# Kernel tuning notes

Hardware: AMD Instinct MI355X
Metric: run time of the kernel (lower is better)

The kernel has to match this reference:

```python
import jax, jax.numpy as jnp
import numpy as np

B, L, IN, D, H = 128, 64, 2, 256, 512  # batch, max_len, input_size, dense_size, hidden_size
A_S2S, A_PTR = H, D  # attention hidden sizes (defaults: hidden_size / dense_size)


def setup_inputs() -> dict:
    key = jax.random.key(0)
    ks = jax.random.split(key, 24)
    s = 0.05
    inp = {
        'inputs': jax.random.normal(ks[0], (B, L, IN), jnp.float32),
        'lengths': jax.random.randint(ks[1], (B,), L // 2, L + 1),
        'targets': jax.random.randint(ks[2], (B, L), 0, L),
        # input_dense: input_size -> dense_size
        'W_in': jax.random.normal(ks[3], (D, IN)) * s,
        'b_in': jnp.zeros((D,)),
        # encoder GRU (input D, hidden H), PyTorch layout [3H, in]
        'enc_Wi': jax.random.normal(ks[4], (3 * H, D)) * s,
        'enc_Wh': jax.random.normal(ks[5], (3 * H, H)) * s,
        'enc_bi': jnp.zeros((3 * H,)),
        'enc_bh': jnp.zeros((3 * H,)),
        # decoder GRU (input D+H, hidden H)
        'dec_Wi': jax.random.normal(ks[6], (3 * H, D + H)) * s,
        'dec_Wh': jax.random.normal(ks[7], (3 * H, H)) * s,
        'dec_bi': jnp.zeros((3 * H,)),
        'dec_bh': jnp.zeros((3 * H,)),
        # Bahdanau seq2seq attention: query_hidden = rnn_layers*H
        's2s_Wq': jax.random.normal(ks[8], (H, A_S2S)) * s,
        's2s_Wk': jax.random.normal(ks[9], (H, A_S2S)) * s,
        's2s_v': jax.random.normal(ks[10], (A_S2S,)) * s,
        # output_dense: hidden -> dense
        'W_out': jax.random.normal(ks[11], (D, H)) * s,
        'b_out': jnp.zeros((D,)),
        # Bahdanau pointer attention over dense_inputs
        'ptr_Wq': jax.random.normal(ks[12], (D, A_PTR)) * s,
        'ptr_Wk': jax.random.normal(ks[13], (D, A_PTR)) * s,
        'ptr_v': jax.random.normal(ks[14], (A_PTR,)) * s,
    }
    return inp


def _gru_cell(x, h, Wi, Wh, bi, bh):
    gi = x @ Wi.T + bi
    gh = h @ Wh.T + bh
    i_r, i_z, i_n = jnp.split(gi, 3, axis=-1)
    h_r, h_z, h_n = jnp.split(gh, 3, axis=-1)
    r = jax.nn.sigmoid(i_r + h_r)
    z = jax.nn.sigmoid(i_z + h_z)
    n = jnp.tanh(i_n + r * h_n)
    return (1.0 - z) * n + z * h


NEG = -1e9


def reference(inputs, lengths, targets, W_in, b_in, enc_Wi, enc_Wh, enc_bi, enc_bh,
              dec_Wi, dec_Wh, dec_bi, dec_bh, s2s_Wq, s2s_Wk, s2s_v,
              W_out, b_out, ptr_Wq, ptr_Wk, ptr_v):
    # teacher_forcing_prob fixed at 1.0 for determinism (uses targets each step)
    dense_inputs = inputs @ W_in.T + b_in            # [B, L, D]
    padding_mask = jnp.arange(L)[None, :] < lengths[:, None]  # [B, L] bool

    # ---- encoder (dynamic_rnn): run GRU over time, take hidden at lengths-1 ----
    def enc_step(h, x_t):
        h2 = _gru_cell(x_t, h, enc_Wi, enc_Wh, enc_bi, enc_bh)
        return h2, h2
    _, hs = jax.lax.scan(enc_step, jnp.zeros((B, H), dense_inputs.dtype),
                         dense_inputs.transpose(1, 0, 2))  # hs: [L, B, H]
    enc_out = hs.transpose(1, 0, 2) * padding_mask[:, :, None]  # zero padded steps
    hidden0 = hs[lengths - 1, jnp.arange(B)]  # final valid hidden, [B, H]

    # Precompute attention key projections (loop-invariant)
    enc_keys = enc_out @ s2s_Wk        # [B, L, A_S2S]
    ptr_keys = dense_inputs @ ptr_Wk   # [B, L, A_PTR]

    def dec_step(carry, inp):
        h, idx, step_mask = carry              # h [B,H], idx [B] int, step_mask [B,L]
        pm_i, tgt_i = inp                      # [B] bool, [B] int
        dec_in = dense_inputs[jnp.arange(B), idx]  # [B, D] gather
        m = pm_i[:, None] & padding_mask           # [B, L]
        # Bahdanau seq2seq attention, query = current hidden state
        q = h @ s2s_Wq                              # [B, A]
        scores = jnp.tanh(q[:, None, :] + enc_keys) @ s2s_v   # [B, L]
        scores = jnp.where(m, scores, NEG)
        w = jax.nn.softmax(scores, axis=-1)
        context = jnp.einsum('bl,blh->bh', w, enc_out)         # [B, H]
        x = jnp.concatenate([context, dec_in], axis=-1)        # [B, H+D]
        h_new = _gru_cell(x, h, dec_Wi, dec_Wh, dec_bi, dec_bh)
        # pointer attention over dense_inputs
        dense_out = h_new @ W_out.T + b_out                    # [B, D]
        p_mask = (step_mask > 0) & m
        pq = dense_out @ ptr_Wq
        plogit = jnp.tanh(pq[:, None, :] + ptr_keys) @ ptr_v   # [B, L]
        plogit = jnp.where(p_mask, plogit, NEG)
        pred = jnp.argmax(plogit, axis=-1)
        next_idx = tgt_i  # teacher forcing
        step_mask_new = step_mask * (1 - jax.nn.one_hot(next_idx, L, dtype=step_mask.dtype))
        return (h_new, next_idx, step_mask_new), (plogit, pred)

    carry0 = (hidden0, jnp.zeros((B,), jnp.int32),
              jnp.ones((B, L), jnp.int32))
    xs = (padding_mask.T, targets.T.astype(jnp.int32))
    _, (logits_t, preds_t) = jax.lax.scan(dec_step, carry0, xs)
    logits = logits_t.transpose(1, 0, 2)       # [B, L, L]
    predictions = preds_t.T                    # [B, L]
    return logits, predictions
```

## Files before the change

kernel.cpp:

```cpp
#include <hip/hip_runtime.h>

#define BB 128
#define LL 64
#define DD 256
#define HH 512
#define NEGC (-1e9f)

#define OFF_DENSE   0
#define OFF_ENCOUT  2097152
#define OFF_ENCKEYS 6291456
#define OFF_PTRKEYS 10485760
#define OFF_X       12582912
#define OFF_HB0     12681216
#define OFF_HB1     12746752
#define OFF_H0      12812288
#define OFF_Q       12877824
#define OFF_PQ      12943360
#define OFF_WQT     12976128
#define OFF_MT      13238272
#define OFF_BQ      13369344
#define OFF_SMASK   13369600

__device__ __forceinline__ float fast_tanh(float x) {
  float e = __expf(2.0f * x);
  return 1.0f - 2.0f / (e + 1.0f);
}
__device__ __forceinline__ float sigmoidf_(float x) {
  return 1.0f / (1.0f + __expf(-x));
}
__device__ __forceinline__ float wsum(float v) {
#pragma unroll
  for (int o = 32; o > 0; o >>= 1) v += __shfl_xor(v, o);
  return v;
}

#define D4(acc) fmaf(xv.x, w.x, fmaf(xv.y, w.y, fmaf(xv.z, w.z, fmaf(xv.w, w.w, acc))))


__global__ __launch_bounds__(256)
void k_init(const float* __restrict__ inp, const float* __restrict__ W_in,
            const float* __restrict__ b_in, float* __restrict__ dense,
            float* __restrict__ hb0, int* __restrict__ smask) {
  int idx = blockIdx.x * 256 + threadIdx.x;
  if (idx < BB * LL * DD) {
    int bl = idx >> 8, d = idx & 255;
    dense[idx] = fmaf(inp[bl * 2], W_in[d * 2], fmaf(inp[bl * 2 + 1], W_in[d * 2 + 1], b_in[d]));
  } else if (idx < BB * LL * DD + BB * HH) {
    hb0[idx - BB * LL * DD] = 0.f;
  } else if (idx < BB * LL * DD + BB * HH + BB * LL) {
    smask[idx - BB * LL * DD - BB * HH] = 1;
  }
}

__global__ __launch_bounds__(256)
void k_tr(const float* __restrict__ Wq, float* __restrict__ Wqt) {
  int idx = blockIdx.x * 256 + threadIdx.x;
  int h = idx >> 9, a = idx & 511;
  Wqt[a * 512 + h] = Wq[idx];
}

__global__ __launch_bounds__(512)
void k_mt(const float* __restrict__ W_out, const float* __restrict__ ptr_Wq,
          const float* __restrict__ b_out, float* __restrict__ Mt, float* __restrict__ bqv) {
  int a = blockIdx.x, tid = threadIdx.x;
  if (a < 256) {
    float acc = 0.f;
    for (int d = 0; d < 256; ++d) acc = fmaf(W_out[d * 512 + tid], ptr_Wq[d * 256 + a], acc);
    Mt[a * 512 + tid] = acc;
  } else if (tid < 256) {
    float acc = 0.f;
    for (int d = 0; d < 256; ++d) acc = fmaf(b_out[d], ptr_Wq[d * 256 + tid], acc);
    bqv[tid] = acc;
  }
}

__global__ __launch_bounds__(256)
void k_ptrkeys(const float* __restrict__ dense, const float* __restrict__ Wk,
               float* __restrict__ keys) {
  __shared__ float s[16 * 256];
  int r0 = blockIdx.x * 16, tid = threadIdx.x;
  for (int idx = tid; idx < 16 * 256; idx += 256) s[idx] = dense[r0 * 256 + idx];
  __syncthreads();
  float acc[16];
#pragma unroll
  for (int ri = 0; ri < 16; ++ri) acc[ri] = 0.f;
  for (int d = 0; d < 256; ++d) {
    float w = Wk[d * 256 + tid];
#pragma unroll
    for (int ri = 0; ri < 16; ++ri) acc[ri] = fmaf(s[ri * 256 + d], w, acc[ri]);
  }
#pragma unroll
  for (int ri = 0; ri < 16; ++ri) keys[(r0 + ri) * 256 + tid] = acc[ri];
}

__global__ __launch_bounds__(512)
void k_enckeys(const float* __restrict__ enc_out, const float* __restrict__ Wk,
               float* __restrict__ keys) {
  __shared__ float s[16 * 512];
  int r0 = blockIdx.x * 16, tid = threadIdx.x;
  for (int idx = tid; idx < 16 * 512; idx += 512) s[idx] = enc_out[r0 * 512 + idx];
  __syncthreads();
  float acc[16];
#pragma unroll
  for (int ri = 0; ri < 16; ++ri) acc[ri] = 0.f;
  for (int h = 0; h < 512; ++h) {
    float w = Wk[h * 512 + tid];
#pragma unroll
    for (int ri = 0; ri < 16; ++ri) acc[ri] = fmaf(s[ri * 512 + h], w, acc[ri]);
  }
#pragma unroll
  for (int ri = 0; ri < 16; ++ri) keys[(r0 + ri) * 512 + tid] = acc[ri];
}

__global__ __launch_bounds__(256)
void k_copy(const float* __restrict__ src, float* __restrict__ dst) {
  int idx = blockIdx.x * 256 + threadIdx.x;
  if (idx < BB * HH) dst[idx] = src[idx];
}

__global__ __launch_bounds__(256)
void k_enc(const float* __restrict__ dense, const float* __restrict__ hin,
           float* __restrict__ hout, const float* __restrict__ Wi,
           const float* __restrict__ Wh, const float* __restrict__ bi,
           const float* __restrict__ bh, const int* __restrict__ lengths,
           float* __restrict__ enc_out, float* __restrict__ h0, int t) {
  __shared__ float xs[16 * 772];
  __shared__ float part[2 * 16 * 8 * 8];
  const int tid = threadIdx.x;
  const int b0 = blockIdx.x * 16, u0 = blockIdx.y * 16;
  for (int idx = tid; idx < 16 * 768; idx += 256) {
    int bl = idx / 768, k = idx - bl * 768;
    xs[bl * 772 + k] = (k < 512) ? hin[(b0 + bl) * 512 + k]
                                 : dense[((b0 + bl) * 64 + t) * 256 + (k - 512)];
  }
  __syncthreads();
  {
    const int b_l = tid & 15, og = (tid >> 4) & 7, kp = tid >> 7;
    const int ua = u0 + og * 2;
    float ar0 = 0, az0 = 0, ain0 = 0, ahn0 = 0, ar1 = 0, az1 = 0, ain1 = 0, ahn1 = 0;
    const float* xr = xs + b_l * 772;
    const int k0 = kp * 384, k1 = k0 + 384;
    const int kA = (k1 < 512) ? k1 : 512;
    for (int k = k0; k < kA; k += 4) {
      float4 xv = *(const float4*)(xr + k);
      float4 w;
      w = *(const float4*)(Wh + (ua) * 512 + k);        ar0  = D4(ar0);
      w = *(const float4*)(Wh + (512 + ua) * 512 + k);  az0  = D4(az0);
      w = *(const float4*)(Wh + (1024 + ua) * 512 + k); ahn0 = D4(ahn0);
      w = *(const float4*)(Wh + (ua + 1) * 512 + k);    ar1  = D4(ar1);
      w = *(const float4*)(Wh + (513 + ua) * 512 + k);  az1  = D4(az1);
      w = *(const float4*)(Wh + (1025 + ua) * 512 + k); ahn1 = D4(ahn1);
    }
    const int kB = (k0 > 512) ? k0 : 512;
    for (int k = kB; k < k1; k += 4) {
      float4 xv = *(const float4*)(xr + k);
      float4 w;
      w = *(const float4*)(Wi + (ua) * 256 + k - 512);        ar0  = D4(ar0);
      w = *(const float4*)(Wi + (512 + ua) * 256 + k - 512);  az0  = D4(az0);
      w = *(const float4*)(Wi + (1024 + ua) * 256 + k - 512); ain0 = D4(ain0);
      w = *(const float4*)(Wi + (ua + 1) * 256 + k - 512);    ar1  = D4(ar1);
      w = *(const float4*)(Wi + (513 + ua) * 256 + k - 512);  az1  = D4(az1);
      w = *(const float4*)(Wi + (1025 + ua) * 256 + k - 512); ain1 = D4(ain1);
    }
    float* pp = part + ((kp * 16 + b_l) * 8 + og) * 8;
    pp[0] = ar0; pp[1] = az0; pp[2] = ain0; pp[3] = ahn0;
    pp[4] = ar1; pp[5] = az1; pp[6] = ain1; pp[7] = ahn1;
  }
  __syncthreads();
  {
    const int b_l = tid & 15, u_l = tid >> 4;
    const int og = u_l >> 1, uu = u_l & 1;
    const float* p0 = part + ((0 * 16 + b_l) * 8 + og) * 8 + uu * 4;
    const float* p1 = part + ((1 * 16 + b_l) * 8 + og) * 8 + uu * 4;
    float ar = p0[0] + p1[0], az = p0[1] + p1[1];
    float ain = p0[2] + p1[2], ahn = p0[3] + p1[3];
    const int u = u0 + u_l, b = b0 + b_l;
    float r = sigmoidf_(ar + bi[u] + bh[u]);
    float z = sigmoidf_(az + bi[512 + u] + bh[512 + u]);
    float n = fast_tanh(ain + bi[1024 + u] + r * (ahn + bh[1024 + u]));
    float hp = xs[b_l * 772 + u];
    float hn = (1.f - z) * n + z * hp;
    hout[b * 512 + u] = hn;
    int lenb = lengths[b];
    enc_out[(b * 64 + t) * 512 + u] = (t < lenb) ? hn : 0.f;
    if (t == lenb - 1) h0[b * 512 + u] = hn;
  }
}

__global__ __launch_bounds__(256)
void k_p1(int step, const float* __restrict__ qbuf, const float* __restrict__ pqbuf,
          const float* __restrict__ enc_keys, const float* __restrict__ ptr_keys,
          const float* __restrict__ enc_out, const float* __restrict__ dense,
          const float* __restrict__ s2s_v, const float* __restrict__ ptr_v,
          const int* __restrict__ lengths, const int* __restrict__ targets,
          int* __restrict__ smask, float* __restrict__ xbuf,
          float* __restrict__ logits, float* __restrict__ preds) {
  __shared__ float sq[512], sv[512], sl[64], wl[64];
  const int b = blockIdx.x, tid = threadIdx.x;
  const int wv = tid >> 6, ln = tid & 63;
  const int lenb = lengths[b];
  if (step > 0) {
    const int j = step - 1;
    sq[tid] = pqbuf[b * 256 + (tid & 255)];
    sv[tid] = ptr_v[tid & 255];
    __syncthreads();
#pragma unroll 4
    for (int li = 0; li < 16; ++li) {
      int l = wv * 16 + li;
      float acc = 0.f;
#pragma unroll
      for (int c = 0; c < 4; ++c) {
        int a = c * 64 + ln;
        acc = fmaf(fast_tanh(sq[a] + ptr_keys[(b * 64 + l) * 256 + a]), sv[a], acc);
      }
      acc = wsum(acc);
      if (ln == 0) sl[l] = acc;
    }
    __syncthreads();
    if (tid < 64) {
      int l = tid;
      bool pm = (j < lenb) && (l < lenb) && (smask[b * 64 + l] != 0);
      float v = pm ? sl[l] : NEGC;
      logits[(b * 64 + j) * 64 + l] = v;
      float bv = v; int bidx = l;
#pragma unroll
      for (int off = 32; off > 0; off >>= 1) {
        float ov = __shfl_xor(bv, off);
        int oi = __shfl_xor(bidx, off);
        if (ov > bv || (ov == bv && oi < bidx)) { bv = ov; bidx = oi; }
      }
      if (l == 0) preds[b * 64 + j] = (float)bidx;
    }
    __syncthreads();
    if (tid == 0) smask[b * 64 + targets[b * 64 + j]] = 0;
    __syncthreads();
  }
  if (step < 64) {
    const int i = step;
    sq[tid] = qbuf[b * 512 + tid];
    sq[tid + 256] = qbuf[b * 512 + 256 + tid];
    sv[tid] = s2s_v[tid];
    sv[tid + 256] = s2s_v[256 + tid];
    __syncthreads();
#pragma unroll 2
    for (int li = 0; li < 16; ++li) {
      int l = wv * 16 + li;
      float acc = 0.f;
#pragma unroll
      for (int c = 0; c < 8; ++c) {
        int a = c * 64 + ln;
        acc = fmaf(fast_tanh(sq[a] + enc_keys[(b * 64 + l) * 512 + a]), sv[a], acc);
      }
      acc = wsum(acc);
      if (ln == 0) sl[l] = ((i < lenb) && (l < lenb)) ? acc : NEGC;
    }
    __syncthreads();
    if (tid < 64) {
      float v = sl[tid];
      float m = v;
#pragma unroll
      for (int off = 32; off > 0; off >>= 1) m = fmaxf(m, __shfl_xor(m, off));
      float e = __expf(v - m);
      float s = e;
#pragma unroll
      for (int off = 32; off > 0; off >>= 1) s += __shfl_xor(s, off);
      wl[tid] = e / s;
    }
    __syncthreads();
    for (int hh = tid; hh < 512; hh += 256) {
      float c = 0.f;
#pragma unroll 8
      for (int l = 0; l < 64; ++l) c = fmaf(wl[l], enc_out[(b * 64 + l) * 512 + hh], c);
      xbuf[b * 768 + hh] = c;
    }
    int idx = (i == 0) ? 0 : targets[b * 64 + i - 1];
    xbuf[b * 768 + 512 + tid] = dense[(b * 64 + idx) * 256 + tid];
  }
}

__global__ __launch_bounds__(256)
void k_p2(const float* __restrict__ xbuf, const float* __restrict__ hin,
          float* __restrict__ hout, const float* __restrict__ Wi,
          const float* __restrict__ Wh, const float* __restrict__ bi,
          const float* __restrict__ bh) {
  __shared__ float xs[8 * 1284];
  __shared__ float part[4 * 8 * 8 * 8];
  const int tid = threadIdx.x;
  const int b0 = blockIdx.x * 8, u0 = blockIdx.y * 16;
  for (int idx = tid; idx < 8 * 1280; idx += 256) {
    int bl = idx / 1280, k = idx - bl * 1280;
    xs[bl * 1284 + k] = (k < 768) ? xbuf[(b0 + bl) * 768 + k]
                                  : hin[(b0 + bl) * 512 + (k - 768)];
  }
  __syncthreads();
  {
    const int b_l = tid & 7, og = (tid >> 3) & 7, kp = tid >> 6;
    const int ua = u0 + og * 2;
    float ar0 = 0, az0 = 0, ain0 = 0, ahn0 = 0, ar1 = 0, az1 = 0, ain1 = 0, ahn1 = 0;
    const float* xr = xs + b_l * 1284;
    const int k0 = kp * 320, k1 = k0 + 320;
    const int kA = (k1 < 768) ? k1 : 768;
    for (int k = k0; k < kA; k += 4) {
      float4 xv = *(const float4*)(xr + k);
      float4 w;
      w = *(const float4*)(Wi + (ua) * 768 + k);        ar0  = D4(ar0);
      w = *(const float4*)(Wi + (512 + ua) * 768 + k);  az0  = D4(az0);
      w = *(const float4*)(Wi + (1024 + ua) * 768 + k); ain0 = D4(ain0);
      w = *(const float4*)(Wi + (ua + 1) * 768 + k);    ar1  = D4(ar1);
      w = *(const float4*)(Wi + (513 + ua) * 768 + k);  az1  = D4(az1);
      w = *(const float4*)(Wi + (1025 + ua) * 768 + k); ain1 = D4(ain1);
    }
    const int kB = (k0 > 768) ? k0 : 768;
    for (int k = kB; k < k1; k += 4) {
      float4 xv = *(const float4*)(xr + k);
      float4 w;
      w = *(const float4*)(Wh + (ua) * 512 + k - 768);        ar0  = D4(ar0);
      w = *(const float4*)(Wh + (512 + ua) * 512 + k - 768);  az0  = D4(az0);
      w = *(const float4*)(Wh + (1024 + ua) * 512 + k - 768); ahn0 = D4(ahn0);
      w = *(const float4*)(Wh + (ua + 1) * 512 + k - 768);    ar1  = D4(ar1);
      w = *(const float4*)(Wh + (513 + ua) * 512 + k - 768);  az1  = D4(az1);
      w = *(const float4*)(Wh + (1025 + ua) * 512 + k - 768); ahn1 = D4(ahn1);
    }
    float* pp = part + ((kp * 8 + b_l) * 8 + og) * 8;
    pp[0] = ar0; pp[1] = az0; pp[2] = ain0; pp[3] = ahn0;
    pp[4] = ar1; pp[5] = az1; pp[6] = ain1; pp[7] = ahn1;
  }
  __syncthreads();
  if (tid < 128) {
    const int b_l = tid & 7, u_l = tid >> 3;
    const int og = u_l >> 1, uu = u_l & 1;
    float ar = 0, az = 0, ain = 0, ahn = 0;
#pragma unroll
    for (int kp = 0; kp < 4; ++kp) {
      const float* p = part + ((kp * 8 + b_l) * 8 + og) * 8 + uu * 4;
      ar += p[0]; az += p[1]; ain += p[2]; ahn += p[3];
    }
    const int u = u0 + u_l, b = b0 + b_l;
    float r = sigmoidf_(ar + bi[u] + bh[u]);
    float z = sigmoidf_(az + bi[512 + u] + bh[512 + u]);
    float n = fast_tanh(ain + bi[1024 + u] + r * (ahn + bh[1024 + u]));
    float hp = xs[b_l * 1284 + 768 + u];
    hout[b * 512 + u] = (1.f - z) * n + z * hp;
  }
}

__global__ __launch_bounds__(256)
void k_p3(const float* __restrict__ hsrc, const float* __restrict__ Wqt,
          const float* __restrict__ Mt, const float* __restrict__ bqv,
          float* __restrict__ qbuf, float* __restrict__ pqbuf) {
  __shared__ float hs[16 * 516];
  __shared__ float part[8 * 16 * 8];
  const int tid = threadIdx.x;
  const int b0 = blockIdx.x * 16, o0 = blockIdx.y * 8;
  for (int idx = tid; idx < 16 * 512; idx += 256) {
    int bl = idx >> 9, k = idx & 511;
    hs[bl * 516 + k] = hsrc[(b0 + bl) * 512 + k];
  }
  __syncthreads();
  {
    const int b_l = tid & 15, og = (tid >> 4) & 1, kp = tid >> 5;
    const int ob = o0 + og * 4;
    const float* w0 = (ob < 512) ? (Wqt + (ob) * 512) : (Mt + (ob - 512) * 512);
    const float* w1 = (ob < 512) ? (Wqt + (ob + 1) * 512) : (Mt + (ob - 511) * 512);
    const float* w2 = (ob < 512) ? (Wqt + (ob + 2) * 512) : (Mt + (ob - 510) * 512);
    const float* w3 = (ob < 512) ? (Wqt + (ob + 3) * 512) : (Mt + (ob - 509) * 512);
    float a0 = 0, a1 = 0, a2 = 0, a3 = 0;
    const float* xr = hs + b_l * 516;
    const int k0 = kp * 64;
    for (int k = k0; k < k0 + 64; k += 4) {
      float4 xv = *(const float4*)(xr + k);
      float4 w;
      w = *(const float4*)(w0 + k); a0 = D4(a0);
      w = *(const float4*)(w1 + k); a1 = D4(a1);
      w = *(const float4*)(w2 + k); a2 = D4(a2);
      w = *(const float4*)(w3 + k); a3 = D4(a3);
    }
    float* pp = part + ((kp * 16 + b_l) * 8 + og * 4);
    pp[0] = a0; pp[1] = a1; pp[2] = a2; pp[3] = a3;
  }
  __syncthreads();
  if (tid < 128) {
    const int b_l = tid & 15, o_l = tid >> 4;
    float s = 0.f;
#pragma unroll
    for (int kp = 0; kp < 8; ++kp) s += part[(kp * 16 + b_l) * 8 + o_l];
    const int b = b0 + b_l, o = o0 + o_l;
    if (o < 512) qbuf[b * 512 + o] = s;
    else pqbuf[b * 256 + (o - 512)] = s + bqv[o - 512];
  }
}

extern "C" void kernel_launch(void* const* d_in, const int* in_sizes, int n_in,
                              void* d_out, int out_size, void* d_ws, size_t ws_size,
                              hipStream_t stream) {
  (void)in_sizes; (void)n_in; (void)out_size; (void)ws_size;
  const float* inputs  = (const float*)d_in[0];
  const int*   lengths = (const int*)d_in[1];
  const int*   targets = (const int*)d_in[2];
  const float* W_in    = (const float*)d_in[3];
  const float* b_in    = (const float*)d_in[4];
  const float* enc_Wi  = (const float*)d_in[5];
  const float* enc_Wh  = (const float*)d_in[6];
  const float* enc_bi  = (const float*)d_in[7];
  const float* enc_bh  = (const float*)d_in[8];
  const float* dec_Wi  = (const float*)d_in[9];
  const float* dec_Wh  = (const float*)d_in[10];
  const float* dec_bi  = (const float*)d_in[11];
  const float* dec_bh  = (const float*)d_in[12];
  const float* s2s_Wq  = (const float*)d_in[13];
  const float* s2s_Wk  = (const float*)d_in[14];
  const float* s2s_v   = (const float*)d_in[15];
  const float* W_out   = (const float*)d_in[16];
  const float* b_out   = (const float*)d_in[17];
  const float* ptr_Wq  = (const float*)d_in[18];
  const float* ptr_Wk  = (const float*)d_in[19];
  const float* ptr_v   = (const float*)d_in[20];

  float* ws = (float*)d_ws;
  float* dense    = ws + OFF_DENSE;
  float* enc_out  = ws + OFF_ENCOUT;
  float* enc_keys = ws + OFF_ENCKEYS;
  float* ptr_keys = ws + OFF_PTRKEYS;
  float* xbuf     = ws + OFF_X;
  float* hb0      = ws + OFF_HB0;
  float* hb1      = ws + OFF_HB1;
  float* h0       = ws + OFF_H0;
  float* qbuf     = ws + OFF_Q;
  float* pqbuf    = ws + OFF_PQ;
  float* Wqt      = ws + OFF_WQT;
  float* Mt       = ws + OFF_MT;
  float* bqv      = ws + OFF_BQ;
  int*   smask    = (int*)(ws + OFF_SMASK);

  float* logits = (float*)d_out;
  float* preds  = (float*)d_out + BB * LL * LL;

  k_init<<<8480, 256, 0, stream>>>(inputs, W_in, b_in, dense, hb0, smask);
  k_tr<<<1024, 256, 0, stream>>>(s2s_Wq, Wqt);
  k_mt<<<257, 512, 0, stream>>>(W_out, ptr_Wq, b_out, Mt, bqv);
  k_ptrkeys<<<512, 256, 0, stream>>>(dense, ptr_Wk, ptr_keys);

  for (int t = 0; t < 64; ++t) {
    float* hi = (t & 1) ? hb1 : hb0;
    float* ho = (t & 1) ? hb0 : hb1;
    k_enc<<<dim3(8, 32), 256, 0, stream>>>(dense, hi, ho, enc_Wi, enc_Wh, enc_bi,
                                           enc_bh, lengths, enc_out, h0, t);
  }
  k_copy<<<256, 256, 0, stream>>>(h0, hb0);
  k_enckeys<<<512, 512, 0, stream>>>(enc_out, s2s_Wk, enc_keys);
  k_p3<<<dim3(8, 96), 256, 0, stream>>>(hb0, Wqt, Mt, bqv, qbuf, pqbuf);

  for (int i = 0; i < 64; ++i) {
    float* hi = (i & 1) ? hb1 : hb0;
    float* ho = (i & 1) ? hb0 : hb1;
    k_p1<<<128, 256, 0, stream>>>(i, qbuf, pqbuf, enc_keys, ptr_keys, enc_out, dense,
                                  s2s_v, ptr_v, lengths, targets, smask, xbuf,
                                  logits, preds);
    k_p2<<<dim3(16, 32), 256, 0, stream>>>(xbuf, hi, ho, dec_Wi, dec_Wh, dec_bi, dec_bh);
    k_p3<<<dim3(8, 96), 256, 0, stream>>>(ho, Wqt, Mt, bqv, qbuf, pqbuf);
  }
  k_p1<<<128, 256, 0, stream>>>(64, qbuf, pqbuf, enc_keys, ptr_keys, enc_out, dense,
                                s2s_v, ptr_v, lengths, targets, smask, xbuf,
                                logits, preds);
}
```

Baseline: 7.112 ms.

## Fuse whole encoder-decoder pipeline into one persistent kernel with grid barriers

Replaces roughly 260 separate kernel launches (encoder steps, attention, GRU, and query projection per decoder step) with one persistent 256-block kernel. Stages are separated by a software grid-wide barrier built on atomics. The decoder query projection is restructured into per-unit-tile partial sums that the next attention phase reduces, which removes a separate projection kernel. This cuts launch overhead and inter-kernel gaps, at the cost of relying on all 256 blocks being co-resident and on the atomic barrier's latency.

```diff
diff --git a/kernel.cpp b/kernel.cpp
--- a/kernel.cpp
+++ b/kernel.cpp
@@ -1,9 +1,5 @@
 #include <hip/hip_runtime.h>
 
-#define BB 128
-#define LL 64
-#define DD 256
-#define HH 512
 #define NEGC (-1e9f)
 
 #define OFF_DENSE   0
@@ -11,15 +7,14 @@
 #define OFF_ENCKEYS 6291456
 #define OFF_PTRKEYS 10485760
 #define OFF_X       12582912
-#define OFF_HB0     12681216
-#define OFF_HB1     12746752
+#define OFF_HA      12681216
+#define OFF_HB      12746752
 #define OFF_H0      12812288
-#define OFF_Q       12877824
-#define OFF_PQ      12943360
-#define OFF_WQT     12976128
-#define OFF_MT      13238272
-#define OFF_BQ      13369344
-#define OFF_SMASK   13369600
+#define OFF_WC      12877824
+#define OFF_BQ      13271040
+#define OFF_QPART   13271296
+#define OFF_SMASK   14844160
+#define OFF_BAR     14852352
 
 __device__ __forceinline__ float fast_tanh(float x) {
   float e = __expf(2.0f * x);
@@ -33,360 +28,416 @@
   for (int o = 32; o > 0; o >>= 1) v += __shfl_xor(v, o);
   return v;
 }
-
 #define D4(acc) fmaf(xv.x, w.x, fmaf(xv.y, w.y, fmaf(xv.z, w.z, fmaf(xv.w, w.w, acc))))
 
+__device__ __forceinline__ void gbar(unsigned* cnt, unsigned* flg, unsigned e) {
+  __syncthreads();
+  if (threadIdx.x == 0) {
+    __threadfence();
+    unsigned prev = __hip_atomic_fetch_add(cnt, 1u, __ATOMIC_ACQ_REL, __HIP_MEMORY_SCOPE_AGENT);
+    if (prev == 256u * e - 1u) {
+      __hip_atomic_store(flg, e, __ATOMIC_RELEASE, __HIP_MEMORY_SCOPE_AGENT);
+    } else {
+      while (__hip_atomic_load(flg, __ATOMIC_ACQUIRE, __HIP_MEMORY_SCOPE_AGENT) < e) {
+        __builtin_amdgcn_s_sleep(2);
+      }
+    }
+  }
+  __syncthreads();
+}
 
 __global__ __launch_bounds__(256)
-void k_init(const float* __restrict__ inp, const float* __restrict__ W_in,
-            const float* __restrict__ b_in, float* __restrict__ dense,
-            float* __restrict__ hb0, int* __restrict__ smask) {
+void k_init2(float* hA, int* smask, unsigned* bar) {
   int idx = blockIdx.x * 256 + threadIdx.x;
-  if (idx < BB * LL * DD) {
+  if (idx < 65536) hA[idx] = 0.f;
+  if (idx < 8192) smask[idx] = 1;
+  if (idx < 2) bar[idx] = 0;
+}
+
+__device__ __forceinline__ void dec_p1(
+    int i, float* sm, int tid, int bid,
+    const float* qpart, const float* bq, const float* enc_keys,
+    const float* ptr_keys, const float* enc_out, const float* dense,
+    const float* sv_g, const float* pv_g, const int* lengths,
+    const int* targets, int* smask, float* xbuf, float* logits, float* preds) {
+  const int wv = tid >> 6, ln = tid & 63;
+  if (bid < 128) {
+    if (i < 64) {
+      const int b = bid;
+      const int lenb = lengths[b];
+      {
+        float s = 0.f;
+#pragma unroll
+        for (int ut = 0; ut < 16; ++ut) s += qpart[(ut * 128 + b) * 768 + tid];
+        sm[tid] = s;
+        sm[512 + tid] = sv_g[tid];
+      }
+      __syncthreads();
+#pragma unroll
+      for (int li = 0; li < 8; ++li) {
+        int l = wv * 8 + li;
+        float acc = 0.f;
+#pragma unroll
+        for (int c = 0; c < 8; ++c) {
+          int a = c * 64 + ln;
+          acc = fmaf(fast_tanh(sm[a] + enc_keys[(b * 64 + l) * 512 + a]), sm[512 + a], acc);
+        }
+        acc = wsum(acc);
+        if (ln == 0) sm[1024 + l] = ((i < lenb) && (l < lenb)) ? acc : NEGC;
+      }
+      __syncthreads();
+      if (tid < 64) {
+        float v = sm[1024 + tid];
+        float m = v;
+#pragma unroll
+        for (int off = 32; off > 0; off >>= 1) m = fmaxf(m, __shfl_xor(m, off));
+        float e = __expf(v - m);
+        float s = e;
+#pragma unroll
+        for (int off = 32; off > 0; off >>= 1) s += __shfl_xor(s, off);
+        sm[1088 + tid] = e / s;
+      }
+      __syncthreads();
+      {
+        float c = 0.f;
+#pragma unroll 8
+        for (int l = 0; l < 64; ++l)
+          c = fmaf(sm[1088 + l], enc_out[(b * 64 + l) * 512 + tid], c);
+        xbuf[b * 768 + tid] = c;
+      }
+      if (tid < 256) {
+        int idx = (i == 0) ? 0 : targets[b * 64 + i - 1];
+        xbuf[b * 768 + 512 + tid] = dense[(b * 64 + idx) * 256 + tid];
+      }
+    }
+  } else {
+    if (i >= 1) {
+      const int b = bid - 128, j = i - 1;
+      const int lenb = lengths[b];
+      if (tid < 256) {
+        float s = 0.f;
+#pragma unroll
+        for (int ut = 0; ut < 16; ++ut) s += qpart[(ut * 128 + b) * 768 + 512 + tid];
+        sm[tid] = s + bq[tid];
+        sm[512 + tid] = pv_g[tid];
+      }
+      __syncthreads();
+#pragma unroll
+      for (int li = 0; li < 8; ++li) {
+        int l = wv * 8 + li;
+        float acc = 0.f;
+#pragma unroll
+        for (int c = 0; c < 4; ++c) {
+          int a = c * 64 + ln;
+          acc = fmaf(fast_tanh(sm[a] + ptr_keys[(b * 64 + l) * 256 + a]), sm[512 + a], acc);
+        }
+        acc = wsum(acc);
+        if (ln == 0) sm[1024 + l] = acc;
+      }
+      __syncthreads();
+      if (tid < 64) {
+        int l = tid;
+        bool pm = (j < lenb) && (l < lenb) && (smask[b * 64 + l] != 0);
+        float v = pm ? sm[1024 + l] : NEGC;
+        logits[(b * 64 + j) * 64 + l] = v;
+        float bv = v; int bidx = l;
+#pragma unroll
+        for (int off = 32; off > 0; off >>= 1) {
+          float ov = __shfl_xor(bv, off);
+          int oi = __shfl_xor(bidx, off);
+          if (ov > bv || (ov == bv && oi < bidx)) { bv = ov; bidx = oi; }
+        }
+        if (l == 0) preds[b * 64 + j] = (float)bidx;
+        if (l == 0) smask[b * 64 + targets[b * 64 + j]] = 0;
+      }
+    }
+  }
+}
+
+__global__ __launch_bounds__(512, 2)
+void k_persist(const float* __restrict__ inp, const int* __restrict__ lengths,
+               const int* __restrict__ targets,
+               const float* __restrict__ W_in, const float* __restrict__ b_in,
+               const float* __restrict__ eWi, const float* __restrict__ eWh,
+               const float* __restrict__ ebi, const float* __restrict__ ebh,
+               const float* __restrict__ dWi, const float* __restrict__ dWh,
+               const float* __restrict__ dbi, const float* __restrict__ dbh,
+               const float* __restrict__ Wq, const float* __restrict__ Wk,
+               const float* __restrict__ sv_g,
+               const float* __restrict__ W_out, const float* __restrict__ b_out,
+               const float* __restrict__ pWq, const float* __restrict__ pWk,
+               const float* __restrict__ pv_g,
+               float* __restrict__ ws, float* __restrict__ logits,
+               float* __restrict__ preds) {
+  __shared__ float sm[14400];
+  float* dense    = ws + OFF_DENSE;
+  float* enc_out  = ws + OFF_ENCOUT;
+  float* enc_keys = ws + OFF_ENCKEYS;
+  float* ptr_keys = ws + OFF_PTRKEYS;
+  float* xbuf     = ws + OFF_X;
+  float* hA       = ws + OFF_HA;
+  float* hB       = ws + OFF_HB;
+  float* h0v      = ws + OFF_H0;
+  float* WC       = ws + OFF_WC;
+  float* bq       = ws + OFF_BQ;
+  float* qpart    = ws + OFF_QPART;
+  int*   smask    = (int*)(ws + OFF_SMASK);
+  unsigned* cnt   = (unsigned*)(ws + OFF_BAR);
+  unsigned* flg   = cnt + 1;
+
+  const int tid = threadIdx.x, bid = blockIdx.x;
+  unsigned ep = 0;
+
+  for (int idx = bid * 8192 + tid; idx < (bid + 1) * 8192; idx += 512) {
     int bl = idx >> 8, d = idx & 255;
-    dense[idx] = fmaf(inp[bl * 2], W_in[d * 2], fmaf(inp[bl * 2 + 1], W_in[d * 2 + 1], b_in[d]));
-  } else if (idx < BB * LL * DD + BB * HH) {
-    hb0[idx - BB * LL * DD] = 0.f;
-  } else if (idx < BB * LL * DD + BB * HH + BB * LL) {
-    smask[idx - BB * LL * DD - BB * HH] = 1;
-  }
-}
-
-__global__ __launch_bounds__(256)
-void k_tr(const float* __restrict__ Wq, float* __restrict__ Wqt) {
-  int idx = blockIdx.x * 256 + threadIdx.x;
-  int h = idx >> 9, a = idx & 511;
-  Wqt[a * 512 + h] = Wq[idx];
-}
-
-__global__ __launch_bounds__(512)
-void k_mt(const float* __restrict__ W_out, const float* __restrict__ ptr_Wq,
-          const float* __restrict__ b_out, float* __restrict__ Mt, float* __restrict__ bqv) {
-  int a = blockIdx.x, tid = threadIdx.x;
-  if (a < 256) {
+    dense[idx] = fmaf(inp[bl * 2], W_in[d * 2],
+                 fmaf(inp[bl * 2 + 1], W_in[d * 2 + 1], b_in[d]));
+  }
+  gbar(cnt, flg, ++ep);
+
+#pragma unroll
+  for (int t2 = 0; t2 < 2; ++t2) {
+    int idx = bid * 1024 + t2 * 512 + tid;
+    int h = idx >> 9, a = idx & 511;
+    WC[h * 768 + a] = Wq[idx];
+  }
+  {
+    int j = bid * 512 + tid;
+    int h = j >> 8, a = j & 255;
     float acc = 0.f;
-    for (int d = 0; d < 256; ++d) acc = fmaf(W_out[d * 512 + tid], ptr_Wq[d * 256 + a], acc);
-    Mt[a * 512 + tid] = acc;
-  } else if (tid < 256) {
+    for (int d = 0; d < 256; ++d)
+      acc = fmaf(W_out[d * 512 + h], pWq[d * 256 + a], acc);
+    WC[h * 768 + 512 + a] = acc;
+  }
+  if (bid == 0 && tid < 256) {
     float acc = 0.f;
-    for (int d = 0; d < 256; ++d) acc = fmaf(b_out[d], ptr_Wq[d * 256 + tid], acc);
-    bqv[tid] = acc;
-  }
-}
-
-__global__ __launch_bounds__(256)
-void k_ptrkeys(const float* __restrict__ dense, const float* __restrict__ Wk,
-               float* __restrict__ keys) {
-  __shared__ float s[16 * 256];
-  int r0 = blockIdx.x * 16, tid = threadIdx.x;
-  for (int idx = tid; idx < 16 * 256; idx += 256) s[idx] = dense[r0 * 256 + idx];
-  __syncthreads();
-  float acc[16];
-#pragma unroll
-  for (int ri = 0; ri < 16; ++ri) acc[ri] = 0.f;
-  for (int d = 0; d < 256; ++d) {
-    float w = Wk[d * 256 + tid];
-#pragma unroll
-    for (int ri = 0; ri < 16; ++ri) acc[ri] = fmaf(s[ri * 256 + d], w, acc[ri]);
-  }
-#pragma unroll
-  for (int ri = 0; ri < 16; ++ri) keys[(r0 + ri) * 256 + tid] = acc[ri];
-}
-
-__global__ __launch_bounds__(512)
-void k_enckeys(const float* __restrict__ enc_out, const float* __restrict__ Wk,
-               float* __restrict__ keys) {
-  __shared__ float s[16 * 512];
-  int r0 = blockIdx.x * 16, tid = threadIdx.x;
-  for (int idx = tid; idx < 16 * 512; idx += 512) s[idx] = enc_out[r0 * 512 + idx];
-  __syncthreads();
-  float acc[16];
-#pragma unroll
-  for (int ri = 0; ri < 16; ++ri) acc[ri] = 0.f;
-  for (int h = 0; h < 512; ++h) {
-    float w = Wk[h * 512 + tid];
-#pragma unroll
-    for (int ri = 0; ri < 16; ++ri) acc[ri] = fmaf(s[ri * 512 + h], w, acc[ri]);
-  }
-#pragma unroll
-  for (int ri = 0; ri < 16; ++ri) keys[(r0 + ri) * 512 + tid] = acc[ri];
-}
-
-__global__ __launch_bounds__(256)
-void k_copy(const float* __restrict__ src, float* __restrict__ dst) {
-  int idx = blockIdx.x * 256 + threadIdx.x;
-  if (idx < BB * HH) dst[idx] = src[idx];
-}
-
-__global__ __launch_bounds__(256)
-void k_enc(const float* __restrict__ dense, const float* __restrict__ hin,
-           float* __restrict__ hout, const float* __restrict__ Wi,
-           const float* __restrict__ Wh, const float* __restrict__ bi,
-           const float* __restrict__ bh, const int* __restrict__ lengths,
-           float* __restrict__ enc_out, float* __restrict__ h0, int t) {
-  __shared__ float xs[16 * 772];
-  __shared__ float part[2 * 16 * 8 * 8];
-  const int tid = threadIdx.x;
-  const int b0 = blockIdx.x * 16, u0 = blockIdx.y * 16;
-  for (int idx = tid; idx < 16 * 768; idx += 256) {
-    int bl = idx / 768, k = idx - bl * 768;
-    xs[bl * 772 + k] = (k < 512) ? hin[(b0 + bl) * 512 + k]
-                                 : dense[((b0 + bl) * 64 + t) * 256 + (k - 512)];
-  }
-  __syncthreads();
+    for (int d = 0; d < 256; ++d) acc = fmaf(b_out[d], pWq[d * 256 + tid], acc);
+    bq[tid] = acc;
+  }
   {
-    const int b_l = tid & 15, og = (tid >> 4) & 7, kp = tid >> 7;
-    const int ua = u0 + og * 2;
-    float ar0 = 0, az0 = 0, ain0 = 0, ahn0 = 0, ar1 = 0, az1 = 0, ain1 = 0, ahn1 = 0;
-    const float* xr = xs + b_l * 772;
-    const int k0 = kp * 384, k1 = k0 + 384;
-    const int kA = (k1 < 512) ? k1 : 512;
-    for (int k = k0; k < kA; k += 4) {
-      float4 xv = *(const float4*)(xr + k);
-      float4 w;
-      w = *(const float4*)(Wh + (ua) * 512 + k);        ar0  = D4(ar0);
-      w = *(const float4*)(Wh + (512 + ua) * 512 + k);  az0  = D4(az0);
-      w = *(const float4*)(Wh + (1024 + ua) * 512 + k); ahn0 = D4(ahn0);
-      w = *(const float4*)(Wh + (ua + 1) * 512 + k);    ar1  = D4(ar1);
-      w = *(const float4*)(Wh + (513 + ua) * 512 + k);  az1  = D4(az1);
-      w = *(const float4*)(Wh + (1025 + ua) * 512 + k); ahn1 = D4(ahn1);
-    }
-    const int kB = (k0 > 512) ? k0 : 512;
-    for (int k = kB; k < k1; k += 4) {
-      float4 xv = *(const float4*)(xr + k);
-      float4 w;
-      w = *(const float4*)(Wi + (ua) * 256 + k - 512);        ar0  = D4(ar0);
-      w = *(const float4*)(Wi + (512 + ua) * 256 + k - 512);  az0  = D4(az0);
-      w = *(const float4*)(Wi + (1024 + ua) * 256 + k - 512); ain0 = D4(ain0);
-      w = *(const float4*)(Wi + (ua + 1) * 256 + k - 512);    ar1  = D4(ar1);
-      w = *(const float4*)(Wi + (513 + ua) * 256 + k - 512);  az1  = D4(az1);
-      w = *(const float4*)(Wi + (1025 + ua) * 256 + k - 512); ain1 = D4(ain1);
-    }
-    float* pp = part + ((kp * 16 + b_l) * 8 + og) * 8;
-    pp[0] = ar0; pp[1] = az0; pp[2] = ain0; pp[3] = ahn0;
-    pp[4] = ar1; pp[5] = az1; pp[6] = ain1; pp[7] = ahn1;
-  }
-  __syncthreads();
+    const int r0 = bid * 32;
+    for (int idx = tid; idx < 32 * 256; idx += 512) {
+      int r = idx >> 8, d = idx & 255;
+      sm[r * 260 + d] = dense[(r0 + r) * 256 + d];
+    }
+    __syncthreads();
+    const int o = tid & 255, rh = tid >> 8;
+    float acc[16];
+#pragma unroll
+    for (int ri = 0; ri < 16; ++ri) acc[ri] = 0.f;
+    for (int d = 0; d < 256; ++d) {
+      float w = pWk[d * 256 + o];
+#pragma unroll
+      for (int ri = 0; ri < 16; ++ri)
+        acc[ri] = fmaf(sm[(rh * 16 + ri) * 260 + d], w, acc[ri]);
+    }
+#pragma unroll
+    for (int ri = 0; ri < 16; ++ri)
+      ptr_keys[(r0 + rh * 16 + ri) * 256 + o] = acc[ri];
+  }
+  gbar(cnt, flg, ++ep);
+
+  const int bt_e = bid >> 5, ut_e = bid & 31;
+  const int b0e = bt_e * 16, u0e = ut_e * 16;
+  for (int t = 0; t < 64; ++t) {
+    const float* hin = (t & 1) ? hB : hA;
+    float* hout      = (t & 1) ? hA : hB;
+    for (int idx = tid; idx < 16 * 512; idx += 512) {
+      int bl = idx >> 9, k = idx & 511;
+      sm[bl * 772 + k] = hin[(b0e + bl) * 512 + k];
+    }
+    for (int idx = tid; idx < 16 * 256; idx += 512) {
+      int bl = idx >> 8, k = idx & 255;
+      sm[bl * 772 + 512 + k] = dense[((b0e + bl) * 64 + t) * 256 + k];
+    }
+    __syncthreads();
+    {
+      const int b_l = tid & 15, u_l = (tid >> 4) & 15, kp = tid >> 8;
+      const int u = u0e + u_l;
+      const float* xr = sm + b_l * 772;
+      float ar = 0, az = 0, ain = 0, ahn = 0;
+      if (kp == 0) {
+        const float* wr = eWh + u * 512;
+        const float* wz = eWh + (512 + u) * 512;
+        const float* wn = eWh + (1024 + u) * 512;
+        for (int k = 0; k < 384; k += 4) {
+          float4 xv = *(const float4*)(xr + k);
+          float4 w;
+          w = *(const float4*)(wr + k); ar  = D4(ar);
+          w = *(const float4*)(wz + k); az  = D4(az);
+          w = *(const float4*)(wn + k); ahn = D4(ahn);
+        }
+      } else {
+        const float* wr = eWh + u * 512;
+        const float* wz = eWh + (512 + u) * 512;
+        const float* wn = eWh + (1024 + u) * 512;
+        for (int k = 384; k < 512; k += 4) {
+          float4 xv = *(const float4*)(xr + k);
+          float4 w;
+          w = *(const float4*)(wr + k); ar  = D4(ar);
+          w = *(const float4*)(wz + k); az  = D4(az);
+          w = *(const float4*)(wn + k); ahn = D4(ahn);
+        }
+        const float* vr = eWi + u * 256;
+        const float* vz = eWi + (512 + u) * 256;
+        const float* vn = eWi + (1024 + u) * 256;
+        for (int k = 0; k < 256; k += 4) {
+          float4 xv = *(const float4*)(xr + 512 + k);
+          float4 w;
+          w = *(const float4*)(vr + k); ar  = D4(ar);
+          w = *(const float4*)(vz + k); az  = D4(az);
+          w = *(const float4*)(vn + k); ain = D4(ain);
+        }
+      }
+      float* pp = sm + 12352 + ((kp * 16 + b_l) * 16 + u_l) * 4;
+      pp[0] = ar; pp[1] = az; pp[2] = ain; pp[3] = ahn;
+    }
+    __syncthreads();
+    if (tid < 256) {
+      const int b_l = tid & 15, u_l = tid >> 4;
+      const float* p0 = sm + 12352 + ((b_l) * 16 + u_l) * 4;
+      const float* p1 = sm + 12352 + ((16 + b_l) * 16 + u_l) * 4;
+      float ar = p0[0] + p1[0], az = p0[1] + p1[1];
+      float ain = p0[2] + p1[2], ahn = p0[3] + p1[3];
+      const int u = u0e + u_l, b = b0e + b_l;
+      float r = sigmoidf_(ar + ebi[u] + ebh[u]);
+      float z = sigmoidf_(az + ebi[512 + u] + ebh[512 + u]);
+      float n = fast_tanh(ain + ebi[1024 + u] + r * (ahn + ebh[1024 + u]));
+      float hp = sm[b_l * 772 + u];
+      float hn = (1.f - z) * n + z * hp;
+      hout[b * 512 + u] = hn;
+      int lenb = lengths[b];
+      enc_out[(b * 64 + t) * 512 + u] = (t < lenb) ? hn : 0.f;
+      if (t == lenb - 1) h0v[b * 512 + u] = hn;
+    }
+    gbar(cnt, flg, ++ep);
+  }
+
+  const int bt_d = bid >> 4, ut_d = bid & 15;
+  const int b0d = bt_d * 8, u0d = ut_d * 32;
+#pragma unroll 1
+  for (int pass = 0; pass < 2; ++pass) {
+    const int r0 = bid * 32 + pass * 16;
+    for (int idx = tid; idx < 16 * 512; idx += 512) {
+      int r = idx >> 9, h = idx & 511;
+      sm[r * 516 + h] = enc_out[(r0 + r) * 512 + h];
+    }
+    __syncthreads();
+    float acc[16];
+#pragma unroll
+    for (int ri = 0; ri < 16; ++ri) acc[ri] = 0.f;
+    for (int h = 0; h < 512; ++h) {
+      float w = Wk[h * 512 + tid];
+#pragma unroll
+      for (int ri = 0; ri < 16; ++ri) acc[ri] = fmaf(sm[ri * 516 + h], w, acc[ri]);
+    }
+#pragma unroll
+    for (int ri = 0; ri < 16; ++ri) enc_keys[(r0 + ri) * 512 + tid] = acc[ri];
+    __syncthreads();
+  }
   {
-    const int b_l = tid & 15, u_l = tid >> 4;
-    const int og = u_l >> 1, uu = u_l & 1;
-    const float* p0 = part + ((0 * 16 + b_l) * 8 + og) * 8 + uu * 4;
-    const float* p1 = part + ((1 * 16 + b_l) * 8 + og) * 8 + uu * 4;
-    float ar = p0[0] + p1[0], az = p0[1] + p1[1];
-    float ain = p0[2] + p1[2], ahn = p0[3] + p1[3];
-    const int u = u0 + u_l, b = b0 + b_l;
-    float r = sigmoidf_(ar + bi[u] + bh[u]);
-    float z = sigmoidf_(az + bi[512 + u] + bh[512 + u]);
-    float n = fast_tanh(ain + bi[1024 + u] + r * (ahn + bh[1024 + u]));
-    float hp = xs[b_l * 772 + u];
-    float hn = (1.f - z) * n + z * hp;
-    hout[b * 512 + u] = hn;
-    int lenb = lengths[b];
-    enc_out[(b * 64 + t) * 512 + u] = (t < lenb) ? hn : 0.f;
-    if (t == lenb - 1) h0[b * 512 + u] = hn;
-  }
-}
-
-__global__ __launch_bounds__(256)
-void k_p1(int step, const float* __restrict__ qbuf, const float* __restrict__ pqbuf,
-          const float* __restrict__ enc_keys, const float* __restrict__ ptr_keys,
-          const float* __restrict__ enc_out, const float* __restrict__ dense,
-          const float* __restrict__ s2s_v, const float* __restrict__ ptr_v,
-          const int* __restrict__ lengths, const int* __restrict__ targets,
-          int* __restrict__ smask, float* __restrict__ xbuf,
-          float* __restrict__ logits, float* __restrict__ preds) {
-  __shared__ float sq[512], sv[512], sl[64], wl[64];
-  const int b = blockIdx.x, tid = threadIdx.x;
-  const int wv = tid >> 6, ln = tid & 63;
-  const int lenb = lengths[b];
-  if (step > 0) {
-    const int j = step - 1;
-    sq[tid] = pqbuf[b * 256 + (tid & 255)];
-    sv[tid] = ptr_v[tid & 255];
-    __syncthreads();
-#pragma unroll 4
-    for (int li = 0; li < 16; ++li) {
-      int l = wv * 16 + li;
-      float acc = 0.f;
-#pragma unroll
-      for (int c = 0; c < 4; ++c) {
-        int a = c * 64 + ln;
-        acc = fmaf(fast_tanh(sq[a] + ptr_keys[(b * 64 + l) * 256 + a]), sv[a], acc);
-      }
-      acc = wsum(acc);
-      if (ln == 0) sl[l] = acc;
-    }
-    __syncthreads();
-    if (tid < 64) {
-      int l = tid;
-      bool pm = (j < lenb) && (l < lenb) && (smask[b * 64 + l] != 0);
-      float v = pm ? sl[l] : NEGC;
-      logits[(b * 64 + j) * 64 + l] = v;
-      float bv = v; int bidx = l;
-#pragma unroll
-      for (int off = 32; off > 0; off >>= 1) {
-        float ov = __shfl_xor(bv, off);
-        int oi = __shfl_xor(bidx, off);
-        if (ov > bv || (ov == bv && oi < bidx)) { bv = ov; bidx = oi; }
-      }
-      if (l == 0) preds[b * 64 + j] = (float)bidx;
-    }
-    __syncthreads();
-    if (tid == 0) smask[b * 64 + targets[b * 64 + j]] = 0;
-    __syncthreads();
-  }
-  if (step < 64) {
-    const int i = step;
-    sq[tid] = qbuf[b * 512 + tid];
-    sq[tid + 256] = qbuf[b * 512 + 256 + tid];
-    sv[tid] = s2s_v[tid];
-    sv[tid + 256] = s2s_v[256 + tid];
-    __syncthreads();
-#pragma unroll 2
-    for (int li = 0; li < 16; ++li) {
-      int l = wv * 16 + li;
-      float acc = 0.f;
-#pragma unroll
-      for (int c = 0; c < 8; ++c) {
-        int a = c * 64 + ln;
-        acc = fmaf(fast_tanh(sq[a] + enc_keys[(b * 64 + l) * 512 + a]), sv[a], acc);
-      }
-      acc = wsum(acc);
-      if (ln == 0) sl[l] = ((i < lenb) && (l < lenb)) ? acc : NEGC;
-    }
-    __syncthreads();
-    if (tid < 64) {
-      float v = sl[tid];
-      float m = v;
-#pragma unroll
-      for (int off = 32; off > 0; off >>= 1) m = fmaxf(m, __shfl_xor(m, off));
-      float e = __expf(v - m);
-      float s = e;
-#pragma unroll
-      for (int off = 32; off > 0; off >>= 1) s += __shfl_xor(s, off);
-      wl[tid] = e / s;
-    }
-    __syncthreads();
-    for (int hh = tid; hh < 512; hh += 256) {
-      float c = 0.f;
-#pragma unroll 8
-      for (int l = 0; l < 64; ++l) c = fmaf(wl[l], enc_out[(b * 64 + l) * 512 + hh], c);
-      xbuf[b * 768 + hh] = c;
-    }
-    int idx = (i == 0) ? 0 : targets[b * 64 + i - 1];
-    xbuf[b * 768 + 512 + tid] = dense[(b * 64 + idx) * 256 + tid];
-  }
-}
-
-__global__ __launch_bounds__(256)
-void k_p2(const float* __restrict__ xbuf, const float* __restrict__ hin,
-          float* __restrict__ hout, const float* __restrict__ Wi,
-          const float* __restrict__ Wh, const float* __restrict__ bi,
-          const float* __restrict__ bh) {
-  __shared__ float xs[8 * 1284];
-  __shared__ float part[4 * 8 * 8 * 8];
-  const int tid = threadIdx.x;
-  const int b0 = blockIdx.x * 8, u0 = blockIdx.y * 16;
-  for (int idx = tid; idx < 8 * 1280; idx += 256) {
-    int bl = idx / 1280, k = idx - bl * 1280;
-    xs[bl * 1284 + k] = (k < 768) ? xbuf[(b0 + bl) * 768 + k]
-                                  : hin[(b0 + bl) * 512 + (k - 768)];
-  }
-  __syncthreads();
-  {
-    const int b_l = tid & 7, og = (tid >> 3) & 7, kp = tid >> 6;
-    const int ua = u0 + og * 2;
-    float ar0 = 0, az0 = 0, ain0 = 0, ahn0 = 0, ar1 = 0, az1 = 0, ain1 = 0, ahn1 = 0;
-    const float* xr = xs + b_l * 1284;
-    const int k0 = kp * 320, k1 = k0 + 320;
-    const int kA = (k1 < 768) ? k1 : 768;
-    for (int k = k0; k < kA; k += 4) {
-      float4 xv = *(const float4*)(xr + k);
-      float4 w;
-      w = *(const float4*)(Wi + (ua) * 768 + k);        ar0  = D4(ar0);
-      w = *(const float4*)(Wi + (512 + ua) * 768 + k);  az0  = D4(az0);
-      w = *(const float4*)(Wi + (1024 + ua) * 768 + k); ain0 = D4(ain0);
-      w = *(const float4*)(Wi + (ua + 1) * 768 + k);    ar1  = D4(ar1);
-      w = *(const float4*)(Wi + (513 + ua) * 768 + k);  az1  = D4(az1);
-      w = *(const float4*)(Wi + (1025 + ua) * 768 + k); ain1 = D4(ain1);
-    }
-    const int kB = (k0 > 768) ? k0 : 768;
-    for (int k = kB; k < k1; k += 4) {
-      float4 xv = *(const float4*)(xr + k);
-      float4 w;
-      w = *(const float4*)(Wh + (ua) * 512 + k - 768);        ar0  = D4(ar0);
-      w = *(const float4*)(Wh + (512 + ua) * 512 + k - 768);  az0  = D4(az0);
-      w = *(const float4*)(Wh + (1024 + ua) * 512 + k - 768); ahn0 = D4(ahn0);
-      w = *(const float4*)(Wh + (ua + 1) * 512 + k - 768);    ar1  = D4(ar1);
-      w = *(const float4*)(Wh + (513 + ua) * 512 + k - 768);  az1  = D4(az1);
-      w = *(const float4*)(Wh + (1025 + ua) * 512 + k - 768); ahn1 = D4(ahn1);
-    }
-    float* pp = part + ((kp * 8 + b_l) * 8 + og) * 8;
-    pp[0] = ar0; pp[1] = az0; pp[2] = ain0; pp[3] = ahn0;
-    pp[4] = ar1; pp[5] = az1; pp[6] = ain1; pp[7] = ahn1;
-  }
-  __syncthreads();
-  if (tid < 128) {
-    const int b_l = tid & 7, u_l = tid >> 3;
-    const int og = u_l >> 1, uu = u_l & 1;
-    float ar = 0, az = 0, ain = 0, ahn = 0;
-#pragma unroll
-    for (int kp = 0; kp < 4; ++kp) {
-      const float* p = part + ((kp * 8 + b_l) * 8 + og) * 8 + uu * 4;
-      ar += p[0]; az += p[1]; ain += p[2]; ahn += p[3];
-    }
-    const int u = u0 + u_l, b = b0 + b_l;
-    float r = sigmoidf_(ar + bi[u] + bh[u]);
-    float z = sigmoidf_(az + bi[512 + u] + bh[512 + u]);
-    float n = fast_tanh(ain + bi[1024 + u] + r * (ahn + bh[1024 + u]));
-    float hp = xs[b_l * 1284 + 768 + u];
-    hout[b * 512 + u] = (1.f - z) * n + z * hp;
-  }
-}
-
-__global__ __launch_bounds__(256)
-void k_p3(const float* __restrict__ hsrc, const float* __restrict__ Wqt,
-          const float* __restrict__ Mt, const float* __restrict__ bqv,
-          float* __restrict__ qbuf, float* __restrict__ pqbuf) {
-  __shared__ float hs[16 * 516];
-  __shared__ float part[8 * 16 * 8];
-  const int tid = threadIdx.x;
-  const int b0 = blockIdx.x * 16, o0 = blockIdx.y * 8;
-  for (int idx = tid; idx < 16 * 512; idx += 256) {
-    int bl = idx >> 9, k = idx & 511;
-    hs[bl * 516 + k] = hsrc[(b0 + bl) * 512 + k];
-  }
-  __syncthreads();
-  {
-    const int b_l = tid & 15, og = (tid >> 4) & 1, kp = tid >> 5;
-    const int ob = o0 + og * 4;
-    const float* w0 = (ob < 512) ? (Wqt + (ob) * 512) : (Mt + (ob - 512) * 512);
-    const float* w1 = (ob < 512) ? (Wqt + (ob + 1) * 512) : (Mt + (ob - 511) * 512);
-    const float* w2 = (ob < 512) ? (Wqt + (ob + 2) * 512) : (Mt + (ob - 510) * 512);
-    const float* w3 = (ob < 512) ? (Wqt + (ob + 3) * 512) : (Mt + (ob - 509) * 512);
-    float a0 = 0, a1 = 0, a2 = 0, a3 = 0;
-    const float* xr = hs + b_l * 516;
-    const int k0 = kp * 64;
-    for (int k = k0; k < k0 + 64; k += 4) {
-      float4 xv = *(const float4*)(xr + k);
-      float4 w;
-      w = *(const float4*)(w0 + k); a0 = D4(a0);
-      w = *(const float4*)(w1 + k); a1 = D4(a1);
-      w = *(const float4*)(w2 + k); a2 = D4(a2);
-      w = *(const float4*)(w3 + k); a3 = D4(a3);
-    }
-    float* pp = part + ((kp * 16 + b_l) * 8 + og * 4);
-    pp[0] = a0; pp[1] = a1; pp[2] = a2; pp[3] = a3;
-  }
-  __syncthreads();
-  if (tid < 128) {
-    const int b_l = tid & 15, o_l = tid >> 4;
-    float s = 0.f;
-#pragma unroll
-    for (int kp = 0; kp < 8; ++kp) s += part[(kp * 16 + b_l) * 8 + o_l];
-    const int b = b0 + b_l, o = o0 + o_l;
-    if (o < 512) qbuf[b * 512 + o] = s;
-    else pqbuf[b * 256 + (o - 512)] = s + bqv[o - 512];
+    if (tid < 256) sm[tid] = h0v[(b0d + (tid >> 5)) * 512 + u0d + (tid & 31)];
+    __syncthreads();
+    for (int o = tid; o < 768; o += 512) {
+      float acc[8];
+#pragma unroll
+      for (int b = 0; b < 8; ++b) acc[b] = 0.f;
+      for (int k = 0; k < 32; ++k) {
+        float w = WC[(u0d + k) * 768 + o];
+#pragma unroll
+        for (int b = 0; b < 8; ++b) acc[b] = fmaf(sm[b * 32 + k], w, acc[b]);
+      }
+#pragma unroll
+      for (int b = 0; b < 8; ++b) qpart[(ut_d * 128 + b0d + b) * 768 + o] = acc[b];
+    }
+  }
+  gbar(cnt, flg, ++ep);
+
+  for (int i = 0; i <= 64; ++i) {
+    dec_p1(i, sm, tid, bid, qpart, bq, enc_keys, ptr_keys, enc_out, dense,
+           sv_g, pv_g, lengths, targets, smask, xbuf, logits, preds);
+    if (i == 64) break;
+    gbar(cnt, flg, ++ep);
+
+    const float* hin = (i == 0) ? h0v : ((i & 1) ? hB : hA);
+    float* hout      = (i & 1) ? hA : hB;
+    for (int idx = tid; idx < 8 * 768; idx += 512) {
+      int bl = idx / 768, k = idx - bl * 768;
+      sm[bl * 1284 + k] = xbuf[(b0d + bl) * 768 + k];
+    }
+    for (int idx = tid; idx < 8 * 512; idx += 512) {
+      int bl = idx >> 9, k = idx & 511;
+      sm[bl * 1284 + 768 + k] = hin[(b0d + bl) * 512 + k];
+    }
+    __syncthreads();
+    {
+      const int b_l = tid & 7, u_l = (tid >> 3) & 31, kp = tid >> 8;
+      const int u = u0d + u_l;
+      const float* xr = sm + b_l * 1284;
+      float ar = 0, az = 0, ain = 0, ahn = 0;
+      const float* wr = dWi + u * 768;
+      const float* wz = dWi + (512 + u) * 768;
+      const float* wn = dWi + (1024 + u) * 768;
+      if (kp == 0) {
+        for (int k = 0; k < 640; k += 4) {
+          float4 xv = *(const float4*)(xr + k);
+          float4 w;
+          w = *(const float4*)(wr + k); ar  = D4(ar);
+          w = *(const float4*)(wz + k); az  = D4(az);
+          w = *(const float4*)(wn + k); ain = D4(ain);
+        }
+      } else {
+        for (int k = 640; k < 768; k += 4) {
+          float4 xv = *(const float4*)(xr + k);
+          float4 w;
+          w = *(const float4*)(wr + k); ar  = D4(ar);
+          w = *(const float4*)(wz + k); az  = D4(az);
+          w = *(const float4*)(wn + k); ain = D4(ain);
+        }
+        const float* hr = dWh + u * 512;
+        const float* hz = dWh + (512 + u) * 512;
+        const float* hn_ = dWh + (1024 + u) * 512;
+        for (int k = 0; k < 512; k += 4) {
+          float4 xv = *(const float4*)(xr + 768 + k);
+          float4 w;
+          w = *(const float4*)(hr + k);  ar  = D4(ar);
+          w = *(const float4*)(hz + k);  az  = D4(az);
+          w = *(const float4*)(hn_ + k); ahn = D4(ahn);
+        }
+      }
+      float* pp = sm + 10272 + ((kp * 8 + b_l) * 32 + u_l) * 4;
+      pp[0] = ar; pp[1] = az; pp[2] = ain; pp[3] = ahn;
+    }
+    __syncthreads();
+    if (tid < 256) {
+      const int b_l = tid & 7, u_l = tid >> 3;
+      const float* p0 = sm + 10272 + ((b_l) * 32 + u_l) * 4;
+      const float* p1 = sm + 10272 + ((8 + b_l) * 32 + u_l) * 4;
+      float ar = p0[0] + p1[0], az = p0[1] + p1[1];
+      float ain = p0[2] + p1[2], ahn = p0[3] + p1[3];
+      const int u = u0d + u_l, b = b0d + b_l;
+      float r = sigmoidf_(ar + dbi[u] + dbh[u]);
+      float z = sigmoidf_(az + dbi[512 + u] + dbh[512 + u]);
+      float n = fast_tanh(ain + dbi[1024 + u] + r * (ahn + dbh[1024 + u]));
+      float hp = sm[b_l * 1284 + 768 + u];
+      float hnv = (1.f - z) * n + z * hp;
+      hout[b * 512 + u] = hnv;
+      sm[12320 + b_l * 32 + u_l] = hnv;
+    }
+    __syncthreads();
+    for (int o = tid; o < 768; o += 512) {
+      float acc[8];
+#pragma unroll
+      for (int b = 0; b < 8; ++b) acc[b] = 0.f;
+      for (int k = 0; k < 32; ++k) {
+        float w = WC[(u0d + k) * 768 + o];
+#pragma unroll
+        for (int b = 0; b < 8; ++b) acc[b] = fmaf(sm[12320 + b * 32 + k], w, acc[b]);
+      }
+#pragma unroll
+      for (int b = 0; b < 8; ++b) qpart[(ut_d * 128 + b0d + b) * 768 + o] = acc[b];
+    }
+    gbar(cnt, flg, ++ep);
   }
 }
 
@@ -417,49 +468,15 @@
   const float* ptr_v   = (const float*)d_in[20];
 
   float* ws = (float*)d_ws;
-  float* dense    = ws + OFF_DENSE;
-  float* enc_out  = ws + OFF_ENCOUT;
-  float* enc_keys = ws + OFF_ENCKEYS;
-  float* ptr_keys = ws + OFF_PTRKEYS;
-  float* xbuf     = ws + OFF_X;
-  float* hb0      = ws + OFF_HB0;
-  float* hb1      = ws + OFF_HB1;
-  float* h0       = ws + OFF_H0;
-  float* qbuf     = ws + OFF_Q;
-  float* pqbuf    = ws + OFF_PQ;
-  float* Wqt      = ws + OFF_WQT;
-  float* Mt       = ws + OFF_MT;
-  float* bqv      = ws + OFF_BQ;
-  int*   smask    = (int*)(ws + OFF_SMASK);
-
   float* logits = (float*)d_out;
-  float* preds  = (float*)d_out + BB * LL * LL;
-
-  k_init<<<8480, 256, 0, stream>>>(inputs, W_in, b_in, dense, hb0, smask);
-  k_tr<<<1024, 256, 0, stream>>>(s2s_Wq, Wqt);
-  k_mt<<<257, 512, 0, stream>>>(W_out, ptr_Wq, b_out, Mt, bqv);
-  k_ptrkeys<<<512, 256, 0, stream>>>(dense, ptr_Wk, ptr_keys);
-
-  for (int t = 0; t < 64; ++t) {
-    float* hi = (t & 1) ? hb1 : hb0;
-    float* ho = (t & 1) ? hb0 : hb1;
-    k_enc<<<dim3(8, 32), 256, 0, stream>>>(dense, hi, ho, enc_Wi, enc_Wh, enc_bi,
-                                           enc_bh, lengths, enc_out, h0, t);
-  }
-  k_copy<<<256, 256, 0, stream>>>(h0, hb0);
-  k_enckeys<<<512, 512, 0, stream>>>(enc_out, s2s_Wk, enc_keys);
-  k_p3<<<dim3(8, 96), 256, 0, stream>>>(hb0, Wqt, Mt, bqv, qbuf, pqbuf);
-
-  for (int i = 0; i < 64; ++i) {
-    float* hi = (i & 1) ? hb1 : hb0;
-    float* ho = (i & 1) ? hb0 : hb1;
-    k_p1<<<128, 256, 0, stream>>>(i, qbuf, pqbuf, enc_keys, ptr_keys, enc_out, dense,
-                                  s2s_v, ptr_v, lengths, targets, smask, xbuf,
-                                  logits, preds);
-    k_p2<<<dim3(16, 32), 256, 0, stream>>>(xbuf, hi, ho, dec_Wi, dec_Wh, dec_bi, dec_bh);
-    k_p3<<<dim3(8, 96), 256, 0, stream>>>(ho, Wqt, Mt, bqv, qbuf, pqbuf);
-  }
-  k_p1<<<128, 256, 0, stream>>>(64, qbuf, pqbuf, enc_keys, ptr_keys, enc_out, dense,
-                                s2s_v, ptr_v, lengths, targets, smask, xbuf,
-                                logits, preds);
-}
+  float* preds  = (float*)d_out + 128 * 64 * 64;
+
+  k_init2<<<256, 256, 0, stream>>>(ws + OFF_HA, (int*)(ws + OFF_SMASK),
+                                   (unsigned*)(ws + OFF_BAR));
+  k_persist<<<256, 512, 0, stream>>>(inputs, lengths, targets, W_in, b_in,
+                                     enc_Wi, enc_Wh, enc_bi, enc_bh,
+                                     dec_Wi, dec_Wh, dec_bi, dec_bh,
+                                     s2s_Wq, s2s_Wk, s2s_v, W_out, b_out,
+                                     ptr_Wq, ptr_Wk, ptr_v,
+                                     ws, logits, preds);
+}
```

After: 26.26 ms. 269% more time.
